# Kernel optimization log

Hardware: AMD Instinct MI355X
Metric: run time of the kernel (lower is better)

## Reference

```python
import jax, jax.numpy as jnp
import numpy as np


def conv1x1(x, w, b):
    # x: [B, Cin, D, H, W], w: [Cout, Cin], b: [Cout]
    return jnp.einsum('bcdhw,oc->bodhw', x, w) + b[None, :, None, None, None]


def setup_inputs() -> dict:
    key = jax.random.key(0)
    ks = jax.random.split(key, 9)
    B, C, D, H, W = 2, 64, 16, 16, 16
    Cc = 64          # context_dim
    C8 = C // 8      # inner attention dim
    s = 0.05
    return {
        'x': jax.random.normal(ks[0], (B, C, D, H, W), jnp.float32),
        'context': jax.random.normal(ks[1], (B, Cc, D, H, W), jnp.float32),
        'Wq': jax.random.normal(ks[2], (C8, C), jnp.float32) * s,
        'bq': jax.random.normal(ks[3], (C8,), jnp.float32) * s,
        'Wk': jax.random.normal(ks[4], (C8, Cc), jnp.float32) * s,
        'bk': jax.random.normal(ks[5], (C8,), jnp.float32) * s,
        'Wv': jax.random.normal(ks[6], (C, Cc), jnp.float32) * s,
        'bv': jax.random.normal(ks[7], (C,), jnp.float32) * s,
        'gamma': jax.random.normal(ks[8], (1,), jnp.float32) * s,
    }


def reference(x, context, Wq, bq, Wk, bk, Wv, bv, gamma):
    B, C, D, H, W = x.shape
    N = D * H * W
    q = conv1x1(x, Wq, bq).reshape(B, -1, N)        # [B, C/8, N]
    k = conv1x1(context, Wk, bk).reshape(B, -1, N)  # [B, C/8, N]
    v = conv1x1(context, Wv, bv).reshape(B, C, N)   # [B, C, N]
    # energy[b, n, m] = q[:, :, n] . k[:, :, m]  (no scaling, as in source)
    energy = jnp.einsum('bcn,bcm->bnm', q, k)       # [B, N, N]
    attn = jax.nn.softmax(energy, axis=-1)
    # out = v @ attn^T : out[b, c, n] = sum_m v[b, c, m] * attn[b, n, m]
    out = jnp.einsum('bcm,bnm->bcn', v, attn).reshape(B, C, D, H, W)
    return gamma[0] * out + x
```

## Files before the change

kernel.cpp:

```cpp
#include <hip/hip_runtime.h>

#define NTOK 4096

typedef __attribute__((ext_vector_type(8))) short short8;
typedef __attribute__((ext_vector_type(4))) float f32x4;
typedef __attribute__((ext_vector_type(4))) unsigned int uint4v;

__device__ __forceinline__ unsigned short f2bf(float f) {
    unsigned u = __float_as_uint(f);
    u += 0x7fffu + ((u >> 16) & 1u);
    return (unsigned short)(u >> 16);
}

__device__ __forceinline__ unsigned int pk2(float lo, float hi) {
    return __builtin_amdgcn_perm(__float_as_uint(hi), __float_as_uint(lo), 0x07060302u);
}

__global__ __launch_bounds__(256) void proj(
    const float* __restrict__ x, const float* __restrict__ ctx,
    const float* __restrict__ Wq, const float* __restrict__ bq,
    const float* __restrict__ Wk, const float* __restrict__ bk,
    const float* __restrict__ Wv, const float* __restrict__ bv,
    unsigned short* __restrict__ qbf, unsigned short* __restrict__ kbf,
    unsigned short* __restrict__ vtp)
{
    __shared__ float sW[16 * 64];
    __shared__ float sB[16];
    int tid  = threadIdx.x;
    int ogrp = blockIdx.z;
    int b    = blockIdx.y;
    int n0   = blockIdx.x * 64;

    if (ogrp == 0) {
        for (int i = tid; i < 1024; i += 256)
            sW[i] = (i < 512) ? Wq[i] : Wk[i - 512];
        if (tid < 16) sB[tid] = (tid < 8) ? bq[tid] : bk[tid - 8];
    } else {
        for (int i = tid; i < 1024; i += 256)
            sW[i] = Wv[(ogrp - 1) * 1024 + i];
        if (tid < 16) sB[tid] = bv[(ogrp - 1) * 16 + tid];
    }
    __syncthreads();

    int nn   = tid & 63;
    int osub = tid >> 6;
    const float* inp = (ogrp == 0 && osub < 2) ? x : ctx;
    const float* ip  = inp + (size_t)b * 64 * NTOK + n0 + nn;

    float a0 = sB[osub * 4 + 0], a1 = sB[osub * 4 + 1];
    float a2 = sB[osub * 4 + 2], a3 = sB[osub * 4 + 3];
#pragma unroll 16
    for (int c = 0; c < 64; ++c) {
        float val = ip[(size_t)c * NTOK];
        a0 += sW[(osub * 4 + 0) * 64 + c] * val;
        a1 += sW[(osub * 4 + 1) * 64 + c] * val;
        a2 += sW[(osub * 4 + 2) * 64 + c] * val;
        a3 += sW[(osub * 4 + 3) * 64 + c] * val;
    }
    float av[4] = {a0, a1, a2, a3};

    if (ogrp == 0) {
        bool isq = osub < 2;
        float sc = isq ? 1.4426950408889634f : 1.0f;
        unsigned short* dst = isq ? qbf : kbf;
        int half = osub & 1;
        ushort4 pk = {f2bf(av[0] * sc), f2bf(av[1] * sc), f2bf(av[2] * sc), f2bf(av[3] * sc)};
        *(ushort4*)&dst[((size_t)b * NTOK + n0 + nn) * 8 + half * 4] = pk;
    } else {
        int cbase = (ogrp - 1) * 16 + osub * 4;
        int m  = n0 + nn;
        int g  = m & ~31;
        int mm = m & 31;
        int p  = ((mm >> 2) & 3) * 8 + (mm >> 4) * 4 + (mm & 3);
#pragma unroll
        for (int j = 0; j < 4; ++j)
            vtp[((size_t)b * 64 + cbase + j) * NTOK + g + p] = f2bf(av[j]);
    }
}

__global__ __launch_bounds__(512, 4) void attn5(
    const unsigned short* __restrict__ qbf, const unsigned short* __restrict__ kbf,
    const unsigned short* __restrict__ vtp,
    float* __restrict__ part)
{
    __shared__ float sO[8][64][17];
    __shared__ float sL[8][16];

    int tid  = threadIdx.x;
    int w    = tid >> 6, lane = tid & 63;
    int n    = lane & 15, quad = lane >> 4;
    int nt   = blockIdx.x;
    int b    = blockIdx.y;
    int qz   = blockIdx.z;
    int n0   = nt * 16;

    const f32x4 z4 = {0.f, 0.f, 0.f, 0.f};
    const short8 z8 = {0, 0, 0, 0, 0, 0, 0, 0};

    short8 bq = z8;
    if (quad == 0)
        bq = *(const short8*)&qbf[((size_t)b * NTOK + n0 + n) * 8];

    const unsigned short* kb = kbf + (size_t)b * NTOK * 8;
    const unsigned short* vb = vtp + (size_t)b * 64 * NTOK;
    int mbase = qz * 1024 + w * 128;

#define KLD(h, t) (quad == 0 ? *(const short8*)&kb[(size_t)(mbase + (h) * 64 + (t) * 16 + n) * 8] : z8)
#define VLD(h, s, ct) (*(const short8*)&vb[(size_t)((ct) * 16 + n) * NTOK + mbase + (h) * 64 + (s) * 32 + quad * 8])

    f32x4 acc0 = z4, acc1 = z4, acc2 = z4, acc3 = z4;
    float lsum = 0.f;

    short8 kf0 = KLD(0, 0), kf1 = KLD(0, 1), kf2 = KLD(0, 2), kf3 = KLD(0, 3);
    short8 af0 = VLD(0, 0, 0), af1 = VLD(0, 0, 1), af2 = VLD(0, 0, 2), af3 = VLD(0, 0, 3);
    short8 af4 = VLD(0, 1, 0), af5 = VLD(0, 1, 1), af6 = VLD(0, 1, 2), af7 = VLD(0, 1, 3);

    for (int h = 0; h < 2; ++h) {
        f32x4 sa0 = __builtin_amdgcn_mfma_f32_16x16x32_bf16(kf0, bq, z4, 0, 0, 0);
        f32x4 sa1 = __builtin_amdgcn_mfma_f32_16x16x32_bf16(kf1, bq, z4, 0, 0, 0);
        f32x4 sa2 = __builtin_amdgcn_mfma_f32_16x16x32_bf16(kf2, bq, z4, 0, 0, 0);
        f32x4 sa3 = __builtin_amdgcn_mfma_f32_16x16x32_bf16(kf3, bq, z4, 0, 0, 0);
        if (h < 1) {
            kf0 = KLD(h + 1, 0); kf1 = KLD(h + 1, 1);
            kf2 = KLD(h + 1, 2); kf3 = KLD(h + 1, 3);
        }

        float e00 = __builtin_amdgcn_exp2f(sa0[0]), e01 = __builtin_amdgcn_exp2f(sa0[1]);
        float e02 = __builtin_amdgcn_exp2f(sa0[2]), e03 = __builtin_amdgcn_exp2f(sa0[3]);
        float e10 = __builtin_amdgcn_exp2f(sa1[0]), e11 = __builtin_amdgcn_exp2f(sa1[1]);
        float e12 = __builtin_amdgcn_exp2f(sa1[2]), e13 = __builtin_amdgcn_exp2f(sa1[3]);
        float e20 = __builtin_amdgcn_exp2f(sa2[0]), e21 = __builtin_amdgcn_exp2f(sa2[1]);
        float e22 = __builtin_amdgcn_exp2f(sa2[2]), e23 = __builtin_amdgcn_exp2f(sa2[3]);
        float e30 = __builtin_amdgcn_exp2f(sa3[0]), e31 = __builtin_amdgcn_exp2f(sa3[1]);
        float e32 = __builtin_amdgcn_exp2f(sa3[2]), e33 = __builtin_amdgcn_exp2f(sa3[3]);
        lsum += ((e00 + e01) + (e02 + e03)) + ((e10 + e11) + (e12 + e13))
              + ((e20 + e21) + (e22 + e23)) + ((e30 + e31) + (e32 + e33));

        uint4v t0, t1;
        t0[0] = pk2(e00, e01); t0[1] = pk2(e02, e03);
        t0[2] = pk2(e10, e11); t0[3] = pk2(e12, e13);
        t1[0] = pk2(e20, e21); t1[1] = pk2(e22, e23);
        t1[2] = pk2(e30, e31); t1[3] = pk2(e32, e33);
        short8 pf0 = __builtin_bit_cast(short8, t0);
        short8 pf1 = __builtin_bit_cast(short8, t1);

        acc0 = __builtin_amdgcn_mfma_f32_16x16x32_bf16(af0, pf0, acc0, 0, 0, 0);
        acc1 = __builtin_amdgcn_mfma_f32_16x16x32_bf16(af1, pf0, acc1, 0, 0, 0);
        acc2 = __builtin_amdgcn_mfma_f32_16x16x32_bf16(af2, pf0, acc2, 0, 0, 0);
        acc3 = __builtin_amdgcn_mfma_f32_16x16x32_bf16(af3, pf0, acc3, 0, 0, 0);
        acc0 = __builtin_amdgcn_mfma_f32_16x16x32_bf16(af4, pf1, acc0, 0, 0, 0);
        acc1 = __builtin_amdgcn_mfma_f32_16x16x32_bf16(af5, pf1, acc1, 0, 0, 0);
        acc2 = __builtin_amdgcn_mfma_f32_16x16x32_bf16(af6, pf1, acc2, 0, 0, 0);
        acc3 = __builtin_amdgcn_mfma_f32_16x16x32_bf16(af7, pf1, acc3, 0, 0, 0);

        if (h < 1) {
            af0 = VLD(h + 1, 0, 0); af1 = VLD(h + 1, 0, 1);
            af2 = VLD(h + 1, 0, 2); af3 = VLD(h + 1, 0, 3);
            af4 = VLD(h + 1, 1, 0); af5 = VLD(h + 1, 1, 1);
            af6 = VLD(h + 1, 1, 2); af7 = VLD(h + 1, 1, 3);
        }
    }
#undef KLD
#undef VLD

    lsum += __shfl_xor(lsum, 16);
    lsum += __shfl_xor(lsum, 32);
    if (lane < 16) sL[w][n] = lsum;
    f32x4 acc[4] = {acc0, acc1, acc2, acc3};
#pragma unroll
    for (int ct = 0; ct < 4; ++ct)
#pragma unroll
        for (int r = 0; r < 4; ++r)
            sO[w][ct * 16 + quad * 4 + r][n] = acc[ct][r];
    __syncthreads();

    float* pb = part + ((size_t)((b * (NTOK / 16) + nt) * 4 + qz)) * 1040;
    for (int i = tid; i < 1040; i += 512) {
        float s = 0.f;
        if (i < 1024) {
            int c = i >> 4, nn2 = i & 15;
#pragma unroll
            for (int w2 = 0; w2 < 8; ++w2) s += sO[w2][c][nn2];
        } else {
            int nn2 = i - 1024;
#pragma unroll
            for (int w2 = 0; w2 < 8; ++w2) s += sL[w2][nn2];
        }
        pb[i] = s;
    }
}

__global__ __launch_bounds__(256) void merge4(
    const float* __restrict__ part, const float* __restrict__ x,
    const float* __restrict__ gamma, float* __restrict__ out)
{
    int tid = threadIdx.x;
    int nt  = blockIdx.x;
    int b   = blockIdx.y;
    int c   = tid >> 2;
    int ns  = (tid & 3) * 4;

    const float* pb = part + ((size_t)((b * (NTOK / 16) + nt) * 4)) * 1040;
    float4 o = {0.f, 0.f, 0.f, 0.f};
    float4 L = {0.f, 0.f, 0.f, 0.f};
#pragma unroll
    for (int qz = 0; qz < 4; ++qz) {
        const float* p = pb + qz * 1040;
        float4 ov = *(const float4*)&p[c * 16 + ns];
        float4 lv = *(const float4*)&p[1024 + ns];
        o.x += ov.x; o.y += ov.y; o.z += ov.z; o.w += ov.w;
        L.x += lv.x; L.y += lv.y; L.z += lv.z; L.w += lv.w;
    }
    float g = gamma[0];
    size_t ob = ((size_t)b * 64 + c) * NTOK + nt * 16 + ns;
    float4 xv = *(const float4*)&x[ob];
    float4 res;
    res.x = g * (o.x / L.x) + xv.x;
    res.y = g * (o.y / L.y) + xv.y;
    res.z = g * (o.z / L.z) + xv.z;
    res.w = g * (o.w / L.w) + xv.w;
    *(float4*)&out[ob] = res;
}

extern "C" void kernel_launch(void* const* d_in, const int* in_sizes, int n_in,
                              void* d_out, int out_size, void* d_ws, size_t ws_size,
                              hipStream_t stream) {
    const float* x     = (const float*)d_in[0];
    const float* ctx   = (const float*)d_in[1];
    const float* Wq    = (const float*)d_in[2];
    const float* bq    = (const float*)d_in[3];
    const float* Wk    = (const float*)d_in[4];
    const float* bk    = (const float*)d_in[5];
    const float* Wv    = (const float*)d_in[6];
    const float* bv    = (const float*)d_in[7];
    const float* gamma = (const float*)d_in[8];
    float* out = (float*)d_out;

    unsigned short* qbf = (unsigned short*)d_ws;
    unsigned short* kbf = qbf + 2 * NTOK * 8;
    unsigned short* vtp = kbf + 2 * NTOK * 8;
    float* part = (float*)(vtp + 2 * 64 * NTOK);

    proj<<<dim3(64, 2, 5), 256, 0, stream>>>(x, ctx, Wq, bq, Wk, bk, Wv, bv, qbf, kbf, vtp);
    attn5<<<dim3(NTOK / 16, 2, 4), 512, 0, stream>>>(qbf, kbf, vtp, part);
    merge4<<<dim3(NTOK / 16, 2), 256, 0, stream>>>(part, x, gamma, out);
}
```

Before: 116.1 us.

## Process 64 queries per attention block to reuse K/V loads across query groups

The attention kernel now handles 64 query tokens per block (four 16-token groups) with 4 waves of 256 keys each, so every K and V fragment loaded from global memory feeds four query groups instead of one. This cuts redundant K/V traffic, the number of partial-sum blocks, and cross-wave reduction work. The cost is many more accumulator registers (16 f32x4 accumulators), lower occupancy (256 threads, min 2 blocks), a larger shared buffer, and the loss of the explicit software prefetch of the next K/V tile. The merge kernel is rewritten to match the new partial layout.

```diff
diff --git a/kernel.cpp b/kernel.cpp
--- a/kernel.cpp
+++ b/kernel.cpp
@@ -78,13 +78,13 @@
     }
 }
 
-__global__ __launch_bounds__(512, 4) void attn5(
+__global__ __launch_bounds__(256, 2) void attn6(
     const unsigned short* __restrict__ qbf, const unsigned short* __restrict__ kbf,
     const unsigned short* __restrict__ vtp,
     float* __restrict__ part)
 {
-    __shared__ float sO[8][64][17];
-    __shared__ float sL[8][16];
+    __shared__ float sO[4][64][64];
+    __shared__ float sL[4][64];
 
     int tid  = threadIdx.x;
     int w    = tid >> 6, lane = tid & 63;
@@ -92,105 +92,108 @@
     int nt   = blockIdx.x;
     int b    = blockIdx.y;
     int qz   = blockIdx.z;
-    int n0   = nt * 16;
+    int n0   = nt * 64;
 
     const f32x4 z4 = {0.f, 0.f, 0.f, 0.f};
     const short8 z8 = {0, 0, 0, 0, 0, 0, 0, 0};
 
-    short8 bq = z8;
-    if (quad == 0)
-        bq = *(const short8*)&qbf[((size_t)b * NTOK + n0 + n) * 8];
+    short8 bq[4];
+#pragma unroll
+    for (int g = 0; g < 4; ++g)
+        bq[g] = (quad == 0)
+            ? *(const short8*)&qbf[((size_t)b * NTOK + n0 + g * 16 + n) * 8]
+            : z8;
 
     const unsigned short* kb = kbf + (size_t)b * NTOK * 8;
     const unsigned short* vb = vtp + (size_t)b * 64 * NTOK;
-    int mbase = qz * 1024 + w * 128;
-
-#define KLD(h, t) (quad == 0 ? *(const short8*)&kb[(size_t)(mbase + (h) * 64 + (t) * 16 + n) * 8] : z8)
-#define VLD(h, s, ct) (*(const short8*)&vb[(size_t)((ct) * 16 + n) * NTOK + mbase + (h) * 64 + (s) * 32 + quad * 8])
-
-    f32x4 acc0 = z4, acc1 = z4, acc2 = z4, acc3 = z4;
-    float lsum = 0.f;
-
-    short8 kf0 = KLD(0, 0), kf1 = KLD(0, 1), kf2 = KLD(0, 2), kf3 = KLD(0, 3);
-    short8 af0 = VLD(0, 0, 0), af1 = VLD(0, 0, 1), af2 = VLD(0, 0, 2), af3 = VLD(0, 0, 3);
-    short8 af4 = VLD(0, 1, 0), af5 = VLD(0, 1, 1), af6 = VLD(0, 1, 2), af7 = VLD(0, 1, 3);
-
-    for (int h = 0; h < 2; ++h) {
-        f32x4 sa0 = __builtin_amdgcn_mfma_f32_16x16x32_bf16(kf0, bq, z4, 0, 0, 0);
-        f32x4 sa1 = __builtin_amdgcn_mfma_f32_16x16x32_bf16(kf1, bq, z4, 0, 0, 0);
-        f32x4 sa2 = __builtin_amdgcn_mfma_f32_16x16x32_bf16(kf2, bq, z4, 0, 0, 0);
-        f32x4 sa3 = __builtin_amdgcn_mfma_f32_16x16x32_bf16(kf3, bq, z4, 0, 0, 0);
-        if (h < 1) {
-            kf0 = KLD(h + 1, 0); kf1 = KLD(h + 1, 1);
-            kf2 = KLD(h + 1, 2); kf3 = KLD(h + 1, 3);
+    int mwbase = qz * 1024 + w * 256;
+
+    f32x4 acc[4][4];
+#pragma unroll
+    for (int g = 0; g < 4; ++g)
+#pragma unroll
+        for (int ct = 0; ct < 4; ++ct) acc[g][ct] = z4;
+    float lsum[4] = {0.f, 0.f, 0.f, 0.f};
+
+    for (int h = 0; h < 4; ++h) {
+        int m0 = mwbase + h * 64;
+
+        short8 kf0 = (quad == 0) ? *(const short8*)&kb[(size_t)(m0 + 0 * 16 + n) * 8] : z8;
+        short8 kf1 = (quad == 0) ? *(const short8*)&kb[(size_t)(m0 + 1 * 16 + n) * 8] : z8;
+        short8 kf2 = (quad == 0) ? *(const short8*)&kb[(size_t)(m0 + 2 * 16 + n) * 8] : z8;
+        short8 kf3 = (quad == 0) ? *(const short8*)&kb[(size_t)(m0 + 3 * 16 + n) * 8] : z8;
+
+        short8 af[2][4];
+#pragma unroll
+        for (int s = 0; s < 2; ++s)
+#pragma unroll
+            for (int ct = 0; ct < 4; ++ct)
+                af[s][ct] = *(const short8*)&vb[(size_t)(ct * 16 + n) * NTOK
+                                                + m0 + s * 32 + quad * 8];
+
+#pragma unroll
+        for (int g = 0; g < 4; ++g) {
+            f32x4 sa0 = __builtin_amdgcn_mfma_f32_16x16x32_bf16(kf0, bq[g], z4, 0, 0, 0);
+            f32x4 sa1 = __builtin_amdgcn_mfma_f32_16x16x32_bf16(kf1, bq[g], z4, 0, 0, 0);
+            f32x4 sa2 = __builtin_amdgcn_mfma_f32_16x16x32_bf16(kf2, bq[g], z4, 0, 0, 0);
+            f32x4 sa3 = __builtin_amdgcn_mfma_f32_16x16x32_bf16(kf3, bq[g], z4, 0, 0, 0);
+
+            float e00 = __builtin_amdgcn_exp2f(sa0[0]), e01 = __builtin_amdgcn_exp2f(sa0[1]);
+            float e02 = __builtin_amdgcn_exp2f(sa0[2]), e03 = __builtin_amdgcn_exp2f(sa0[3]);
+            float e10 = __builtin_amdgcn_exp2f(sa1[0]), e11 = __builtin_amdgcn_exp2f(sa1[1]);
+            float e12 = __builtin_amdgcn_exp2f(sa1[2]), e13 = __builtin_amdgcn_exp2f(sa1[3]);
+            float e20 = __builtin_amdgcn_exp2f(sa2[0]), e21 = __builtin_amdgcn_exp2f(sa2[1]);
+            float e22 = __builtin_amdgcn_exp2f(sa2[2]), e23 = __builtin_amdgcn_exp2f(sa2[3]);
+            float e30 = __builtin_amdgcn_exp2f(sa3[0]), e31 = __builtin_amdgcn_exp2f(sa3[1]);
+            float e32 = __builtin_amdgcn_exp2f(sa3[2]), e33 = __builtin_amdgcn_exp2f(sa3[3]);
+            lsum[g] += ((e00 + e01) + (e02 + e03)) + ((e10 + e11) + (e12 + e13))
+                     + ((e20 + e21) + (e22 + e23)) + ((e30 + e31) + (e32 + e33));
+
+            uint4v t0, t1;
+            t0[0] = pk2(e00, e01); t0[1] = pk2(e02, e03);
+            t0[2] = pk2(e10, e11); t0[3] = pk2(e12, e13);
+            t1[0] = pk2(e20, e21); t1[1] = pk2(e22, e23);
+            t1[2] = pk2(e30, e31); t1[3] = pk2(e32, e33);
+            short8 pf0 = __builtin_bit_cast(short8, t0);
+            short8 pf1 = __builtin_bit_cast(short8, t1);
+
+            acc[g][0] = __builtin_amdgcn_mfma_f32_16x16x32_bf16(af[0][0], pf0, acc[g][0], 0, 0, 0);
+            acc[g][1] = __builtin_amdgcn_mfma_f32_16x16x32_bf16(af[0][1], pf0, acc[g][1], 0, 0, 0);
+            acc[g][2] = __builtin_amdgcn_mfma_f32_16x16x32_bf16(af[0][2], pf0, acc[g][2], 0, 0, 0);
+            acc[g][3] = __builtin_amdgcn_mfma_f32_16x16x32_bf16(af[0][3], pf0, acc[g][3], 0, 0, 0);
+            acc[g][0] = __builtin_amdgcn_mfma_f32_16x16x32_bf16(af[1][0], pf1, acc[g][0], 0, 0, 0);
+            acc[g][1] = __builtin_amdgcn_mfma_f32_16x16x32_bf16(af[1][1], pf1, acc[g][1], 0, 0, 0);
+            acc[g][2] = __builtin_amdgcn_mfma_f32_16x16x32_bf16(af[1][2], pf1, acc[g][2], 0, 0, 0);
+            acc[g][3] = __builtin_amdgcn_mfma_f32_16x16x32_bf16(af[1][3], pf1, acc[g][3], 0, 0, 0);
         }
-
-        float e00 = __builtin_amdgcn_exp2f(sa0[0]), e01 = __builtin_amdgcn_exp2f(sa0[1]);
-        float e02 = __builtin_amdgcn_exp2f(sa0[2]), e03 = __builtin_amdgcn_exp2f(sa0[3]);
-        float e10 = __builtin_amdgcn_exp2f(sa1[0]), e11 = __builtin_amdgcn_exp2f(sa1[1]);
-        float e12 = __builtin_amdgcn_exp2f(sa1[2]), e13 = __builtin_amdgcn_exp2f(sa1[3]);
-        float e20 = __builtin_amdgcn_exp2f(sa2[0]), e21 = __builtin_amdgcn_exp2f(sa2[1]);
-        float e22 = __builtin_amdgcn_exp2f(sa2[2]), e23 = __builtin_amdgcn_exp2f(sa2[3]);
-        float e30 = __builtin_amdgcn_exp2f(sa3[0]), e31 = __builtin_amdgcn_exp2f(sa3[1]);
-        float e32 = __builtin_amdgcn_exp2f(sa3[2]), e33 = __builtin_amdgcn_exp2f(sa3[3]);
-        lsum += ((e00 + e01) + (e02 + e03)) + ((e10 + e11) + (e12 + e13))
-              + ((e20 + e21) + (e22 + e23)) + ((e30 + e31) + (e32 + e33));
-
-        uint4v t0, t1;
-        t0[0] = pk2(e00, e01); t0[1] = pk2(e02, e03);
-        t0[2] = pk2(e10, e11); t0[3] = pk2(e12, e13);
-        t1[0] = pk2(e20, e21); t1[1] = pk2(e22, e23);
-        t1[2] = pk2(e30, e31); t1[3] = pk2(e32, e33);
-        short8 pf0 = __builtin_bit_cast(short8, t0);
-        short8 pf1 = __builtin_bit_cast(short8, t1);
-
-        acc0 = __builtin_amdgcn_mfma_f32_16x16x32_bf16(af0, pf0, acc0, 0, 0, 0);
-        acc1 = __builtin_amdgcn_mfma_f32_16x16x32_bf16(af1, pf0, acc1, 0, 0, 0);
-        acc2 = __builtin_amdgcn_mfma_f32_16x16x32_bf16(af2, pf0, acc2, 0, 0, 0);
-        acc3 = __builtin_amdgcn_mfma_f32_16x16x32_bf16(af3, pf0, acc3, 0, 0, 0);
-        acc0 = __builtin_amdgcn_mfma_f32_16x16x32_bf16(af4, pf1, acc0, 0, 0, 0);
-        acc1 = __builtin_amdgcn_mfma_f32_16x16x32_bf16(af5, pf1, acc1, 0, 0, 0);
-        acc2 = __builtin_amdgcn_mfma_f32_16x16x32_bf16(af6, pf1, acc2, 0, 0, 0);
-        acc3 = __builtin_amdgcn_mfma_f32_16x16x32_bf16(af7, pf1, acc3, 0, 0, 0);
-
-        if (h < 1) {
-            af0 = VLD(h + 1, 0, 0); af1 = VLD(h + 1, 0, 1);
-            af2 = VLD(h + 1, 0, 2); af3 = VLD(h + 1, 0, 3);
-            af4 = VLD(h + 1, 1, 0); af5 = VLD(h + 1, 1, 1);
-            af6 = VLD(h + 1, 1, 2); af7 = VLD(h + 1, 1, 3);
-        }
-    }
-#undef KLD
-#undef VLD
-
-    lsum += __shfl_xor(lsum, 16);
-    lsum += __shfl_xor(lsum, 32);
-    if (lane < 16) sL[w][n] = lsum;
-    f32x4 acc[4] = {acc0, acc1, acc2, acc3};
-#pragma unroll
-    for (int ct = 0; ct < 4; ++ct)
-#pragma unroll
-        for (int r = 0; r < 4; ++r)
-            sO[w][ct * 16 + quad * 4 + r][n] = acc[ct][r];
+    }
+
+#pragma unroll
+    for (int g = 0; g < 4; ++g) {
+        float l = lsum[g];
+        l += __shfl_xor(l, 16);
+        l += __shfl_xor(l, 32);
+        if (lane < 16) sL[w][g * 16 + n] = l;
+    }
+#pragma unroll
+    for (int g = 0; g < 4; ++g)
+#pragma unroll
+        for (int ct = 0; ct < 4; ++ct)
+#pragma unroll
+            for (int r = 0; r < 4; ++r)
+                sO[w][ct * 16 + quad * 4 + r][g * 16 + n] = acc[g][ct][r];
     __syncthreads();
 
-    float* pb = part + ((size_t)((b * (NTOK / 16) + nt) * 4 + qz)) * 1040;
-    for (int i = tid; i < 1040; i += 512) {
-        float s = 0.f;
-        if (i < 1024) {
-            int c = i >> 4, nn2 = i & 15;
-#pragma unroll
-            for (int w2 = 0; w2 < 8; ++w2) s += sO[w2][c][nn2];
-        } else {
-            int nn2 = i - 1024;
-#pragma unroll
-            for (int w2 = 0; w2 < 8; ++w2) s += sL[w2][nn2];
-        }
-        pb[i] = s;
-    }
-}
-
-__global__ __launch_bounds__(256) void merge4(
+    float* pb = part + ((size_t)((b * 64 + nt) * 4 + qz)) * 4160;
+    for (int i = tid; i < 4096; i += 256) {
+        int c = i >> 6, nn2 = i & 63;
+        pb[i] = sO[0][c][nn2] + sO[1][c][nn2] + sO[2][c][nn2] + sO[3][c][nn2];
+    }
+    if (tid < 64)
+        pb[4096 + tid] = sL[0][tid] + sL[1][tid] + sL[2][tid] + sL[3][tid];
+}
+
+__global__ __launch_bounds__(256) void mergeq(
     const float* __restrict__ part, const float* __restrict__ x,
     const float* __restrict__ gamma, float* __restrict__ out)
 {
@@ -198,28 +201,32 @@
     int nt  = blockIdx.x;
     int b   = blockIdx.y;
     int c   = tid >> 2;
-    int ns  = (tid & 3) * 4;
-
-    const float* pb = part + ((size_t)((b * (NTOK / 16) + nt) * 4)) * 1040;
-    float4 o = {0.f, 0.f, 0.f, 0.f};
-    float4 L = {0.f, 0.f, 0.f, 0.f};
-#pragma unroll
-    for (int qz = 0; qz < 4; ++qz) {
-        const float* p = pb + qz * 1040;
-        float4 ov = *(const float4*)&p[c * 16 + ns];
-        float4 lv = *(const float4*)&p[1024 + ns];
-        o.x += ov.x; o.y += ov.y; o.z += ov.z; o.w += ov.w;
-        L.x += lv.x; L.y += lv.y; L.z += lv.z; L.w += lv.w;
-    }
+    int j   = tid & 3;
+
+    const float* pb = part + ((size_t)((b * 64 + nt) * 4)) * 4160;
     float g = gamma[0];
-    size_t ob = ((size_t)b * 64 + c) * NTOK + nt * 16 + ns;
-    float4 xv = *(const float4*)&x[ob];
-    float4 res;
-    res.x = g * (o.x / L.x) + xv.x;
-    res.y = g * (o.y / L.y) + xv.y;
-    res.z = g * (o.z / L.z) + xv.z;
-    res.w = g * (o.w / L.w) + xv.w;
-    *(float4*)&out[ob] = res;
+#pragma unroll
+    for (int nq = 0; nq < 4; ++nq) {
+        int ns = j * 16 + nq * 4;
+        float4 o = {0.f, 0.f, 0.f, 0.f};
+        float4 L = {0.f, 0.f, 0.f, 0.f};
+#pragma unroll
+        for (int qz = 0; qz < 4; ++qz) {
+            const float* p = pb + qz * 4160;
+            float4 ov = *(const float4*)&p[c * 64 + ns];
+            float4 lv = *(const float4*)&p[4096 + ns];
+            o.x += ov.x; o.y += ov.y; o.z += ov.z; o.w += ov.w;
+            L.x += lv.x; L.y += lv.y; L.z += lv.z; L.w += lv.w;
+        }
+        size_t ob = ((size_t)b * 64 + c) * NTOK + nt * 64 + ns;
+        float4 xv = *(const float4*)&x[ob];
+        float4 res;
+        res.x = g * (o.x / L.x) + xv.x;
+        res.y = g * (o.y / L.y) + xv.y;
+        res.z = g * (o.z / L.z) + xv.z;
+        res.w = g * (o.w / L.w) + xv.w;
+        *(float4*)&out[ob] = res;
+    }
 }
 
 extern "C" void kernel_launch(void* const* d_in, const int* in_sizes, int n_in,
@@ -242,6 +249,6 @@
     float* part = (float*)(vtp + 2 * 64 * NTOK);
 
     proj<<<dim3(64, 2, 5), 256, 0, stream>>>(x, ctx, Wq, bq, Wk, bk, Wv, bv, qbf, kbf, vtp);
-    attn5<<<dim3(NTOK / 16, 2, 4), 512, 0, stream>>>(qbf, kbf, vtp, part);
-    merge4<<<dim3(NTOK / 16, 2), 256, 0, stream>>>(part, x, gamma, out);
-}
+    attn6<<<dim3(NTOK / 64, 2, 4), 256, 0, stream>>>(qbf, kbf, vtp, part);
+    mergeq<<<dim3(NTOK / 64, 2), 256, 0, stream>>>(part, x, gamma, out);
+}
```

New measurement: 111.4 us. 4.1% less time.
